# Optimization experiments

Hardware: AMD Instinct MI355X
Metric: run time of the kernel (lower is better)

The kernel has to match this reference:

```python
import jax, jax.numpy as jnp
import numpy as np
from math import sqrt

C = 64        # res_channels
LAYERS = 30
CYCLE = 10
T = 1000
B = 16
L = 32768


def setup_inputs() -> dict:
    key = jax.random.key(0)
    ks = jax.random.split(key, 12)

    def p(k, shape):
        return jax.random.normal(k, shape, dtype=jnp.float32) * 0.05

    # DiffusionEmbedding._build_embedding(T+1): table[s, 2d] = cos(s*10^(4d/63)), table[s,2d+1]=sin(...)
    steps = np.arange(T + 1, dtype=np.float64)[:, None]           # [T+1, 1]
    ang = steps * 10.0 ** (np.arange(64)[None, :] * 4.0 / 63.0)   # [T+1, 64]
    emb_table = jnp.asarray(
        np.stack([np.cos(ang), np.sin(ang)], axis=-1).reshape(T + 1, 128),
        dtype=jnp.float32,
    )

    return {
        "audio": jax.random.normal(ks[0], (B, L), dtype=jnp.float32),
        "diffusion_step": jax.random.randint(ks[1], (B,), 0, T),
        "emb_table": emb_table,                      # [T+1, 128]
        "W1": p(ks[2], (512, 128)), "b1": jnp.zeros((512,), jnp.float32),
        "W2": p(ks[3], (512, 512)), "b2": jnp.zeros((512,), jnp.float32),
        "Win": p(ks[4], (C,)),      "bin_": jnp.zeros((C,), jnp.float32),   # 1x1 conv 1->C
        "diff_W": p(ks[5], (LAYERS, C, 512)),   "diff_b": jnp.zeros((LAYERS, C), jnp.float32),
        "dconv_W": p(ks[6], (LAYERS, 2 * C, C, 3)), "dconv_b": jnp.zeros((LAYERS, 2 * C), jnp.float32),
        "out_W": p(ks[7], (LAYERS, 2 * C, C)),  "out_b": jnp.zeros((LAYERS, 2 * C), jnp.float32),
        "Wo1": p(ks[8], (C, C)),    "bo1": jnp.zeros((C,), jnp.float32),
        "Wo2": p(ks[9], (1, C)),    "bo2": jnp.zeros((1,), jnp.float32),
    }


def _dilated_conv(x, w, d):
    # x: [B, C, L], w: [2C, C, 3], 'same' padding with dilation d
    return jax.lax.conv_general_dilated(
        x, w, window_strides=(1,), padding=[(d, d)], rhs_dilation=(d,),
        dimension_numbers=("NCH", "OIH", "NCH"))


def reference(audio, diffusion_step, emb_table, W1, b1, W2, b2, Win, bin_,
              diff_W, diff_b, dconv_W, dconv_b, out_W, out_b, Wo1, bo1, Wo2, bo2):
    # input projection: Conv1d(1, C, 1) + ReLU
    x = jax.nn.relu(audio[:, None, :] * Win[None, :, None] + bin_[None, :, None])  # [B, C, L]

    t = emb_table[diffusion_step]                  # [B, 128]
    t = jax.nn.silu(t @ W1.T + b1)                 # [B, 512]
    t = jax.nn.silu(t @ W2.T + b2)                 # [B, 512]

    skip = jnp.zeros_like(x)
    for i in range(LAYERS):
        d = 2 ** (i % CYCLE)
        dp = jnp.einsum("bk,ck->bc", t, diff_W[i]) + diff_b[i]          # [B, C]
        y = _dilated_conv(x + dp[:, :, None], dconv_W[i], d)
        y = y + dconv_b[i][None, :, None]                                # [B, 2C, L]
        y = jnp.tanh(y[:, :C]) * jax.nn.sigmoid(y[:, C:])                # gated activation [B, C, L]
        z = jnp.einsum("oc,bcl->bol", out_W[i], y) + out_b[i][None, :, None]  # [B, 2C, L]
        x = (x + z[:, :C]) / sqrt(2.0)
        skip = skip + z[:, C:]

    h = skip / sqrt(float(LAYERS))
    h = jax.nn.relu(jnp.einsum("oc,bcl->bol", Wo1, h) + bo1[None, :, None])
    out = jnp.einsum("oc,bcl->bol", Wo2, h) + bo2[None, :, None]         # [B, 1, L]
    return out[:, 0, :]                                                  # [B, L]
```

## Files before the change

kernel.cpp:

```cpp
#include <hip/hip_runtime.h>
#include <hip/hip_bf16.h>
#include <math.h>
#include <stdint.h>

#define NLAYERS 30
#define BB 16
#define LL 32768

#define SS 16384.0f
#define SSI (1.0f / 16384.0f)

typedef __attribute__((ext_vector_type(8))) short bf16x8;
typedef __attribute__((ext_vector_type(8))) short s16x8;
typedef __attribute__((ext_vector_type(4))) float f32x4;

__device__ inline float bf2f(ushort u) {
    union { uint i; float f; } v; v.i = ((uint)u) << 16; return v.f;
}
__device__ inline ushort f2bf(float f) {
    uint u = __float_as_uint(f);
    return (ushort)((u + 0x7FFFu + ((u >> 16) & 1u)) >> 16);
}

__global__ void emb_kernel(const int* __restrict__ step, const float* __restrict__ emb,
                           const float* __restrict__ W1, const float* __restrict__ b1,
                           const float* __restrict__ W2, const float* __restrict__ b2,
                           float* __restrict__ t_out) {
    int b = blockIdx.x, j = threadIdx.x;
    __shared__ float e[128];
    __shared__ float t1[512];
    int s = step[b];
    if (j < 128) e[j] = emb[s * 128 + j];
    __syncthreads();
    float acc = b1[j];
    const float* w = W1 + j * 128;
    for (int k = 0; k < 128; ++k) acc += w[k] * e[k];
    t1[j] = acc / (1.f + __expf(-acc));
    __syncthreads();
    float acc2 = b2[j];
    const float* w2 = W2 + j * 512;
    for (int k = 0; k < 512; ++k) acc2 += w2[k] * t1[k];
    t_out[b * 512 + j] = acc2 / (1.f + __expf(-acc2));
}

__global__ void dp_kernel(const float* __restrict__ t, const float* __restrict__ diff_W,
                          const float* __restrict__ diff_b, float* __restrict__ dp) {
    int i = blockIdx.x, b = blockIdx.y, c = threadIdx.x;
    __shared__ float ts[512];
    for (int k = c; k < 512; k += 64) ts[k] = t[b * 512 + k];
    __syncthreads();
    const float* w = diff_W + (size_t)(i * 64 + c) * 512;
    float acc = diff_b[i * 64 + c];
    for (int k = 0; k < 512; ++k) acc += w[k] * ts[k];
    dp[(i * BB + b) * 64 + c] = acc;
}

__global__ void prep_w_kernel(const float* __restrict__ dconv_W, ushort* __restrict__ wB,
                              const float* __restrict__ out_W, ushort* __restrict__ oB,
                              const float* __restrict__ Wo1, ushort* __restrict__ Wo1B) {
    int idx = blockIdx.x * 256 + threadIdx.x;
    if (idx < 30 * 8 * 6 * 512) {
        int i = idx / 24576;
        int r = idx % 24576;
        int mt = r / 3072;
        int s = (r / 512) % 6;
        int lane = (r >> 3) & 63;
        int j = r & 7;
        int o = mt * 16 + (lane & 15);
        int tap = s >> 1;
        int c = (s & 1) * 32 + (lane >> 4) * 8 + j;
        wB[idx] = f2bf(dconv_W[((size_t)(i * 128 + o) * 64 + c) * 3 + tap]);
    }
    if (idx < 30 * 8 * 2 * 512) {
        int i = idx / 8192;
        int r = idx % 8192;
        int mt = r / 1024;
        int s = (r / 512) % 2;
        int lane = (r >> 3) & 63;
        int j = r & 7;
        int o = mt * 16 + (lane & 15);
        int c = s * 32 + (lane >> 4) * 8 + j;
        oB[idx] = f2bf(out_W[(size_t)(i * 128 + o) * 64 + c]);
    }
    if (idx < 4 * 2 * 512) {
        int mt = idx / 1024;
        int s = (idx / 512) % 2;
        int lane = (idx >> 3) & 63;
        int j = idx & 7;
        int o = mt * 16 + (lane & 15);
        int c = s * 32 + (lane >> 4) * 8 + j;
        const float hscale = SSI * 0.18257418583505537115f;
        Wo1B[idx] = f2bf(Wo1[o * 64 + c] * hscale);
    }
}

__global__ void bias3_kernel(const float* __restrict__ dp, const float* __restrict__ dconv_W,
                             const float* __restrict__ dconv_b, float* __restrict__ bias3) {
    int i = blockIdx.x, b = blockIdx.y, o = threadIdx.x;
    __shared__ float sdp[64];
    if (o < 64) sdp[o] = dp[(i * BB + b) * 64 + o];
    __syncthreads();
    const float* wrow = dconv_W + (size_t)(i * 128 + o) * 192;
    float f = 0.f, lft = 0.f, rgt = 0.f;
    for (int c = 0; c < 64; ++c) {
        float w0 = wrow[c * 3 + 0], w1 = wrow[c * 3 + 1], w2 = wrow[c * 3 + 2];
        float dv = sdp[c];
        f += dv * (w0 + w1 + w2);
        lft += dv * w0;
        rgt += dv * w2;
    }
    float* dst = bias3 + (size_t)(i * BB + b) * 384;
    dst[o] = f + dconv_b[i * 128 + o];
    dst[128 + o] = lft;
    dst[256 + o] = rgt;
}

__global__ void inproj_kernel(const float* __restrict__ audio, const float* __restrict__ Win,
                              const float* __restrict__ bin_, ushort* __restrict__ x) {
    int idx = blockIdx.x * 256 + threadIdx.x;
    int c8 = idx & 7;
    int l = (idx >> 3) & (LL - 1);
    int b = idx >> 18;
    float a = audio[(size_t)b * LL + l];
    ushort us[8];
    #pragma unroll
    for (int cc = 0; cc < 8; ++cc) {
        int c = c8 * 8 + cc;
        float v = a * Win[c] + bin_[c];
        us[cc] = f2bf(v > 0.f ? v : 0.f);
    }
    ushort4* dst = (ushort4*)(x + ((size_t)b * LL + l) * 64 + c8 * 8);
    dst[0] = make_ushort4(us[0], us[1], us[2], us[3]);
    dst[1] = make_ushort4(us[4], us[5], us[6], us[7]);
}

__global__ __launch_bounds__(256) void layer_fused(
    const ushort* __restrict__ xin, ushort* __restrict__ xout, int16_t* __restrict__ skip,
    const ushort* __restrict__ wB,
    const ushort* __restrict__ oB,
    const float* __restrict__ bias3,
    const float* __restrict__ out_b,
    int d) {
    __shared__ __align__(16) ushort su[2][16][72];

    const int b = blockIdx.y;
    const int seg = blockIdx.x;
    const int tid = threadIdx.x;
    const int lane = tid & 63;
    const int p = tid >> 6;
    const int n = lane & 15;
    const int kg = lane >> 4;
    const int rlo = p * 16 + kg * 4;

    bf16x8 A0[6], A1[6], P0[2], P1[2];
    #pragma unroll
    for (int s = 0; s < 6; ++s) {
        A0[s] = *(const bf16x8*)(wB + ((size_t)(p * 6 + s) * 64 + lane) * 8);
        A1[s] = *(const bf16x8*)(wB + ((size_t)((p + 4) * 6 + s) * 64 + lane) * 8);
    }
    #pragma unroll
    for (int s = 0; s < 2; ++s) {
        P0[s] = *(const bf16x8*)(oB + ((size_t)(p * 2 + s) * 64 + lane) * 8);
        P1[s] = *(const bf16x8*)(oB + ((size_t)((p + 4) * 2 + s) * 64 + lane) * 8);
    }
    const float* bb = bias3 + (size_t)b * 384;
    f32x4 bF_lo = *(const f32x4*)(bb + rlo);
    f32x4 bF_hi = *(const f32x4*)(bb + 64 + rlo);
    f32x4 bL_lo = *(const f32x4*)(bb + 128 + rlo);
    f32x4 bL_hi = *(const f32x4*)(bb + 192 + rlo);
    f32x4 bR_lo = *(const f32x4*)(bb + 256 + rlo);
    f32x4 bR_hi = *(const f32x4*)(bb + 320 + rlo);
    f32x4 obL = *(const f32x4*)(out_b + rlo);
    f32x4 obH = *(const f32x4*)(out_b + 64 + rlo);

    const ushort* xb = xin + (size_t)b * LL * 64;
    ushort* xo = xout + (size_t)b * LL * 64;
    int16_t* sb = skip + (size_t)b * LL * 64;
    const float inv_s2 = 0.70710678118654752440f;

    for (int t = 0; t < 32; ++t) {
        const int l0 = seg * 512 + t * 16;
        bf16x8 Bf[6];
        #pragma unroll
        for (int tap = 0; tap < 3; ++tap) {
            int lx = l0 + n + (tap - 1) * d;
            bool v = (lx >= 0) && (lx < LL);
            #pragma unroll
            for (int h = 0; h < 2; ++h) {
                bf16x8 bv = {0, 0, 0, 0, 0, 0, 0, 0};
                if (v) bv = *(const bf16x8*)(xb + (size_t)lx * 64 + h * 32 + kg * 8);
                Bf[tap * 2 + h] = bv;
            }
        }
        f32x4 accL = {0.f, 0.f, 0.f, 0.f}, accH = {0.f, 0.f, 0.f, 0.f};
        #pragma unroll
        for (int s = 0; s < 6; ++s) {
            accL = __builtin_amdgcn_mfma_f32_16x16x32_bf16(A0[s], Bf[s], accL, 0, 0, 0);
            accH = __builtin_amdgcn_mfma_f32_16x16x32_bf16(A1[s], Bf[s], accH, 0, 0, 0);
        }
        int lx0 = l0 + n;
        float selL = (lx0 < d) ? 1.f : 0.f;
        float selR = (lx0 >= LL - d) ? 1.f : 0.f;
        ushort4 uq;
        #pragma unroll
        for (int j = 0; j < 4; ++j) {
            float lo = accL[j] + bF_lo[j] - selL * bL_lo[j] - selR * bR_lo[j];
            float hi = accH[j] + bF_hi[j] - selL * bL_hi[j] - selR * bR_hi[j];
            float tv = 1.f - 2.f / (1.f + __expf(2.f * lo));
            float sv = 1.f / (1.f + __expf(-hi));
            ushort q = f2bf(tv * sv);
            if (j == 0) uq.x = q;
            if (j == 1) uq.y = q;
            if (j == 2) uq.z = q;
            if (j == 3) uq.w = q;
        }
        *(ushort4*)&su[t & 1][n][rlo] = uq;
        __syncthreads();
        bf16x8 Bp[2];
        #pragma unroll
        for (int s = 0; s < 2; ++s)
            Bp[s] = *(const bf16x8*)&su[t & 1][n][s * 32 + kg * 8];
        f32x4 zL = {0.f, 0.f, 0.f, 0.f}, zH = {0.f, 0.f, 0.f, 0.f};
        #pragma unroll
        for (int s = 0; s < 2; ++s) {
            zL = __builtin_amdgcn_mfma_f32_16x16x32_bf16(P0[s], Bp[s], zL, 0, 0, 0);
            zH = __builtin_amdgcn_mfma_f32_16x16x32_bf16(P1[s], Bp[s], zH, 0, 0, 0);
        }
        size_t off = (size_t)lx0 * 64 + rlo;
        ushort4 xv = *(const ushort4*)(xb + off);
        ushort4 xn;
        xn.x = f2bf((bf2f(xv.x) + zL[0] + obL[0]) * inv_s2);
        xn.y = f2bf((bf2f(xv.y) + zL[1] + obL[1]) * inv_s2);
        xn.z = f2bf((bf2f(xv.z) + zL[2] + obL[2]) * inv_s2);
        xn.w = f2bf((bf2f(xv.w) + zL[3] + obL[3]) * inv_s2);
        *(ushort4*)(xo + off) = xn;
        short4 so = *(const short4*)(sb + off);
        short4 sn;
        float v;
        v = fminf(fmaxf((float)so.x * SSI + zH[0] + obH[0], -1.999f), 1.999f);
        sn.x = (short)__float2int_rn(v * SS);
        v = fminf(fmaxf((float)so.y * SSI + zH[1] + obH[1], -1.999f), 1.999f);
        sn.y = (short)__float2int_rn(v * SS);
        v = fminf(fmaxf((float)so.z * SSI + zH[2] + obH[2], -1.999f), 1.999f);
        sn.z = (short)__float2int_rn(v * SS);
        v = fminf(fmaxf((float)so.w * SSI + zH[3] + obH[3], -1.999f), 1.999f);
        sn.w = (short)__float2int_rn(v * SS);
        *(short4*)(sb + off) = sn;
    }
}

__global__ __launch_bounds__(256) void head_mfma(const int16_t* __restrict__ skip,
                                                 const ushort* __restrict__ Wo1B,
                                                 const float* __restrict__ bo1,
                                                 const float* __restrict__ Wo2,
                                                 const float* __restrict__ bo2,
                                                 float* __restrict__ out) {
    const int b = blockIdx.y;
    const int seg = blockIdx.x;
    const int tid = threadIdx.x;
    const int lane = tid & 63;
    const int w = tid >> 6;
    const int n = lane & 15;
    const int kg = lane >> 4;

    bf16x8 A[4][2];
    #pragma unroll
    for (int mt = 0; mt < 4; ++mt)
        #pragma unroll
        for (int s = 0; s < 2; ++s)
            A[mt][s] = *(const bf16x8*)(Wo1B + ((size_t)(mt * 2 + s) * 64 + lane) * 8);
    f32x4 bo1v[4], wo2v[4];
    #pragma unroll
    for (int mt = 0; mt < 4; ++mt) {
        bo1v[mt] = *(const f32x4*)(bo1 + mt * 16 + kg * 4);
        wo2v[mt] = *(const f32x4*)(Wo2 + mt * 16 + kg * 4);
    }
    const float bo2v = bo2[0];
    const int16_t* sb = skip + (size_t)b * LL * 64;

    for (int t = 0; t < 16; ++t) {
        const int l0 = seg * 1024 + t * 64 + w * 16;
        bf16x8 BH[2], BL[2];
        #pragma unroll
        for (int s = 0; s < 2; ++s) {
            s16x8 v = *(const s16x8*)(sb + (size_t)(l0 + n) * 64 + s * 32 + kg * 8);
            bf16x8 bh, bl;
            #pragma unroll
            for (int e = 0; e < 8; ++e) {
                int sv = (int)v[e];
                int h8 = sv >> 8;
                int l8 = sv - (h8 << 8);
                bh[e] = (short)f2bf((float)h8);
                bl[e] = (short)f2bf((float)l8);
            }
            BH[s] = bh;
            BL[s] = bl;
        }
        f32x4 aH[4], aL[4];
        #pragma unroll
        for (int mt = 0; mt < 4; ++mt) {
            aH[mt] = (f32x4){0.f, 0.f, 0.f, 0.f};
            aL[mt] = (f32x4){0.f, 0.f, 0.f, 0.f};
            #pragma unroll
            for (int s = 0; s < 2; ++s) {
                aH[mt] = __builtin_amdgcn_mfma_f32_16x16x32_bf16(A[mt][s], BH[s], aH[mt], 0, 0, 0);
                aL[mt] = __builtin_amdgcn_mfma_f32_16x16x32_bf16(A[mt][s], BL[s], aL[mt], 0, 0, 0);
            }
        }
        float partial = 0.f;
        #pragma unroll
        for (int mt = 0; mt < 4; ++mt) {
            #pragma unroll
            for (int j = 0; j < 4; ++j) {
                float h = aH[mt][j] * 256.f + aL[mt][j] + bo1v[mt][j];
                partial += (h > 0.f ? h : 0.f) * wo2v[mt][j];
            }
        }
        partial += __shfl_xor(partial, 16, 64);
        partial += __shfl_xor(partial, 32, 64);
        if (kg == 0) out[(size_t)b * LL + l0 + n] = partial + bo2v;
    }
}

extern "C" void kernel_launch(void* const* d_in, const int* in_sizes, int n_in,
                              void* d_out, int out_size, void* d_ws, size_t ws_size,
                              hipStream_t stream) {
    const float* audio = (const float*)d_in[0];
    const int* dstep = (const int*)d_in[1];
    const float* emb = (const float*)d_in[2];
    const float* W1 = (const float*)d_in[3];
    const float* b1 = (const float*)d_in[4];
    const float* W2 = (const float*)d_in[5];
    const float* b2 = (const float*)d_in[6];
    const float* Win = (const float*)d_in[7];
    const float* bin_ = (const float*)d_in[8];
    const float* diff_W = (const float*)d_in[9];
    const float* diff_b = (const float*)d_in[10];
    const float* dconv_W = (const float*)d_in[11];
    const float* dconv_b = (const float*)d_in[12];
    const float* out_W = (const float*)d_in[13];
    const float* out_b = (const float*)d_in[14];
    const float* Wo1 = (const float*)d_in[15];
    const float* bo1 = (const float*)d_in[16];
    const float* Wo2 = (const float*)d_in[17];
    const float* bo2 = (const float*)d_in[18];

    const size_t NACT = (size_t)BB * LL * 64;

    uint8_t* p = (uint8_t*)d_ws;
    ushort* x0 = (ushort*)p;     p += NACT * 2;
    ushort* x1 = (ushort*)p;     p += NACT * 2;
    int16_t* skip = (int16_t*)p; p += NACT * 2;
    float* t = (float*)p;        p += 8192 * 4;
    float* dp = (float*)p;       p += 30720 * 4;
    float* bias3 = (float*)p;    p += 184320 * 4;
    ushort* wB = (ushort*)p;     p += 737280 * 2;
    ushort* oB = (ushort*)p;     p += 245760 * 2;
    ushort* Wo1B = (ushort*)p;   p += 4096 * 2;

    hipMemsetAsync(skip, 0, NACT * 2, stream);
    emb_kernel<<<BB, 512, 0, stream>>>(dstep, emb, W1, b1, W2, b2, t);
    dp_kernel<<<dim3(NLAYERS, BB), 64, 0, stream>>>(t, diff_W, diff_b, dp);
    prep_w_kernel<<<2880, 256, 0, stream>>>(dconv_W, wB, out_W, oB, Wo1, Wo1B);
    bias3_kernel<<<dim3(NLAYERS, BB), 128, 0, stream>>>(dp, dconv_W, dconv_b, bias3);
    inproj_kernel<<<16384, 256, 0, stream>>>(audio, Win, bin_, x0);

    dim3 lgrid(LL / 512, BB);
    ushort* xin = x0;
    ushort* xout = x1;
    for (int i = 0; i < NLAYERS; ++i) {
        int d = 1 << (i % 10);
        layer_fused<<<lgrid, 256, 0, stream>>>(
            xin, xout, skip, wB + (size_t)i * 24576, oB + (size_t)i * 8192,
            bias3 + (size_t)i * BB * 384, out_b + i * 128, d);
        ushort* tmp = xin; xin = xout; xout = tmp;
    }
    head_mfma<<<dim3(LL / 1024, BB), 256, 0, stream>>>(skip, Wo1B, bo1, Wo2, bo2,
                                                       (float*)d_out);
}
```

Baseline: 5.272 ms.

## Software-pipeline layer loads with double buffering and halve segment length

```diff
diff --git a/kernel.cpp b/kernel.cpp
--- a/kernel.cpp
+++ b/kernel.cpp
@@ -6,6 +6,8 @@
 #define NLAYERS 30
 #define BB 16
 #define LL 32768
+#define SEG 256
+#define NT (SEG / 16)
 
 #define SS 16384.0f
 #define SSI (1.0f / 16384.0f)
@@ -178,75 +180,101 @@
     int16_t* sb = skip + (size_t)b * LL * 64;
     const float inv_s2 = 0.70710678118654752440f;
 
-    for (int t = 0; t < 32; ++t) {
-        const int l0 = seg * 512 + t * 16;
-        bf16x8 Bf[6];
-        #pragma unroll
-        for (int tap = 0; tap < 3; ++tap) {
-            int lx = l0 + n + (tap - 1) * d;
-            bool v = (lx >= 0) && (lx < LL);
-            #pragma unroll
-            for (int h = 0; h < 2; ++h) {
-                bf16x8 bv = {0, 0, 0, 0, 0, 0, 0, 0};
-                if (v) bv = *(const bf16x8*)(xb + (size_t)lx * 64 + h * 32 + kg * 8);
-                Bf[tap * 2 + h] = bv;
-            }
-        }
-        f32x4 accL = {0.f, 0.f, 0.f, 0.f}, accH = {0.f, 0.f, 0.f, 0.f};
-        #pragma unroll
-        for (int s = 0; s < 6; ++s) {
-            accL = __builtin_amdgcn_mfma_f32_16x16x32_bf16(A0[s], Bf[s], accL, 0, 0, 0);
-            accH = __builtin_amdgcn_mfma_f32_16x16x32_bf16(A1[s], Bf[s], accH, 0, 0, 0);
-        }
-        int lx0 = l0 + n;
-        float selL = (lx0 < d) ? 1.f : 0.f;
-        float selR = (lx0 >= LL - d) ? 1.f : 0.f;
-        ushort4 uq;
-        #pragma unroll
-        for (int j = 0; j < 4; ++j) {
-            float lo = accL[j] + bF_lo[j] - selL * bL_lo[j] - selR * bR_lo[j];
-            float hi = accH[j] + bF_hi[j] - selL * bL_hi[j] - selR * bR_hi[j];
-            float tv = 1.f - 2.f / (1.f + __expf(2.f * lo));
-            float sv = 1.f / (1.f + __expf(-hi));
-            ushort q = f2bf(tv * sv);
-            if (j == 0) uq.x = q;
-            if (j == 1) uq.y = q;
-            if (j == 2) uq.z = q;
-            if (j == 3) uq.w = q;
-        }
-        *(ushort4*)&su[t & 1][n][rlo] = uq;
-        __syncthreads();
-        bf16x8 Bp[2];
-        #pragma unroll
-        for (int s = 0; s < 2; ++s)
-            Bp[s] = *(const bf16x8*)&su[t & 1][n][s * 32 + kg * 8];
-        f32x4 zL = {0.f, 0.f, 0.f, 0.f}, zH = {0.f, 0.f, 0.f, 0.f};
-        #pragma unroll
-        for (int s = 0; s < 2; ++s) {
-            zL = __builtin_amdgcn_mfma_f32_16x16x32_bf16(P0[s], Bp[s], zL, 0, 0, 0);
-            zH = __builtin_amdgcn_mfma_f32_16x16x32_bf16(P1[s], Bp[s], zH, 0, 0, 0);
-        }
-        size_t off = (size_t)lx0 * 64 + rlo;
-        ushort4 xv = *(const ushort4*)(xb + off);
-        ushort4 xn;
-        xn.x = f2bf((bf2f(xv.x) + zL[0] + obL[0]) * inv_s2);
-        xn.y = f2bf((bf2f(xv.y) + zL[1] + obL[1]) * inv_s2);
-        xn.z = f2bf((bf2f(xv.z) + zL[2] + obL[2]) * inv_s2);
-        xn.w = f2bf((bf2f(xv.w) + zL[3] + obL[3]) * inv_s2);
-        *(ushort4*)(xo + off) = xn;
-        short4 so = *(const short4*)(sb + off);
-        short4 sn;
-        float v;
-        v = fminf(fmaxf((float)so.x * SSI + zH[0] + obH[0], -1.999f), 1.999f);
-        sn.x = (short)__float2int_rn(v * SS);
-        v = fminf(fmaxf((float)so.y * SSI + zH[1] + obH[1], -1.999f), 1.999f);
-        sn.y = (short)__float2int_rn(v * SS);
-        v = fminf(fmaxf((float)so.z * SSI + zH[2] + obH[2], -1.999f), 1.999f);
-        sn.z = (short)__float2int_rn(v * SS);
-        v = fminf(fmaxf((float)so.w * SSI + zH[3] + obH[3], -1.999f), 1.999f);
-        sn.w = (short)__float2int_rn(v * SS);
-        *(short4*)(sb + off) = sn;
-    }
+#define LOADB(DST, TT)                                                           \
+    {                                                                            \
+        const int l0_ = seg * SEG + (TT) * 16;                                   \
+        _Pragma("unroll")                                                        \
+        for (int tap = 0; tap < 3; ++tap) {                                      \
+            int lx = l0_ + n + (tap - 1) * d;                                    \
+            bool v = (lx >= 0) && (lx < LL);                                     \
+            _Pragma("unroll")                                                    \
+            for (int h = 0; h < 2; ++h) {                                        \
+                bf16x8 bv = {0, 0, 0, 0, 0, 0, 0, 0};                            \
+                if (v) bv = *(const bf16x8*)(xb + (size_t)lx * 64 + h * 32 + kg * 8); \
+                DST[tap * 2 + h] = bv;                                           \
+            }                                                                    \
+        }                                                                        \
+    }
+
+#define LOADE(XV, SO, TT)                                                        \
+    {                                                                            \
+        size_t off_ = (size_t)(seg * SEG + (TT) * 16 + n) * 64 + rlo;            \
+        XV = *(const ushort4*)(xb + off_);                                       \
+        SO = *(const short4*)(sb + off_);                                        \
+    }
+
+#define BODY(TT, BUF, BF, XV, SO)                                                \
+    {                                                                            \
+        f32x4 accL = {0.f, 0.f, 0.f, 0.f}, accH = {0.f, 0.f, 0.f, 0.f};          \
+        _Pragma("unroll")                                                        \
+        for (int s = 0; s < 6; ++s) {                                            \
+            accL = __builtin_amdgcn_mfma_f32_16x16x32_bf16(A0[s], BF[s], accL, 0, 0, 0); \
+            accH = __builtin_amdgcn_mfma_f32_16x16x32_bf16(A1[s], BF[s], accH, 0, 0, 0); \
+        }                                                                        \
+        const int lx0 = seg * SEG + (TT) * 16 + n;                               \
+        float selL = (lx0 < d) ? 1.f : 0.f;                                      \
+        float selR = (lx0 >= LL - d) ? 1.f : 0.f;                                \
+        ushort4 uq;                                                              \
+        _Pragma("unroll")                                                        \
+        for (int j = 0; j < 4; ++j) {                                            \
+            float lo = accL[j] + bF_lo[j] - selL * bL_lo[j] - selR * bR_lo[j];   \
+            float hi = accH[j] + bF_hi[j] - selL * bL_hi[j] - selR * bR_hi[j];   \
+            float tv = 1.f - 2.f / (1.f + __expf(2.f * lo));                     \
+            float sv = 1.f / (1.f + __expf(-hi));                                \
+            ushort q = f2bf(tv * sv);                                            \
+            if (j == 0) uq.x = q;                                                \
+            if (j == 1) uq.y = q;                                                \
+            if (j == 2) uq.z = q;                                                \
+            if (j == 3) uq.w = q;                                                \
+        }                                                                        \
+        *(ushort4*)&su[BUF][n][rlo] = uq;                                        \
+        asm volatile("s_waitcnt lgkmcnt(0)" ::: "memory");                       \
+        __builtin_amdgcn_s_barrier();                                            \
+        asm volatile("" ::: "memory");                                           \
+        bf16x8 Bp0 = *(const bf16x8*)&su[BUF][n][kg * 8];                        \
+        bf16x8 Bp1 = *(const bf16x8*)&su[BUF][n][32 + kg * 8];                   \
+        f32x4 zL = {0.f, 0.f, 0.f, 0.f}, zH = {0.f, 0.f, 0.f, 0.f};              \
+        zL = __builtin_amdgcn_mfma_f32_16x16x32_bf16(P0[0], Bp0, zL, 0, 0, 0);   \
+        zH = __builtin_amdgcn_mfma_f32_16x16x32_bf16(P1[0], Bp0, zH, 0, 0, 0);   \
+        zL = __builtin_amdgcn_mfma_f32_16x16x32_bf16(P0[1], Bp1, zL, 0, 0, 0);   \
+        zH = __builtin_amdgcn_mfma_f32_16x16x32_bf16(P1[1], Bp1, zH, 0, 0, 0);   \
+        size_t off = (size_t)lx0 * 64 + rlo;                                     \
+        ushort4 xn;                                                              \
+        xn.x = f2bf((bf2f(XV.x) + zL[0] + obL[0]) * inv_s2);                     \
+        xn.y = f2bf((bf2f(XV.y) + zL[1] + obL[1]) * inv_s2);                     \
+        xn.z = f2bf((bf2f(XV.z) + zL[2] + obL[2]) * inv_s2);                     \
+        xn.w = f2bf((bf2f(XV.w) + zL[3] + obL[3]) * inv_s2);                     \
+        *(ushort4*)(xo + off) = xn;                                              \
+        short4 sn;                                                               \
+        float v;                                                                 \
+        v = fminf(fmaxf((float)SO.x * SSI + zH[0] + obH[0], -1.999f), 1.999f);   \
+        sn.x = (short)__float2int_rn(v * SS);                                    \
+        v = fminf(fmaxf((float)SO.y * SSI + zH[1] + obH[1], -1.999f), 1.999f);   \
+        sn.y = (short)__float2int_rn(v * SS);                                    \
+        v = fminf(fmaxf((float)SO.z * SSI + zH[2] + obH[2], -1.999f), 1.999f);   \
+        sn.z = (short)__float2int_rn(v * SS);                                    \
+        v = fminf(fmaxf((float)SO.w * SSI + zH[3] + obH[3], -1.999f), 1.999f);   \
+        sn.w = (short)__float2int_rn(v * SS);                                    \
+        *(short4*)(sb + off) = sn;                                               \
+    }
+
+    bf16x8 FA[6], FB[6];
+    ushort4 xvA, xvB;
+    short4 soA, soB;
+    LOADB(FA, 0)
+    LOADE(xvA, soA, 0)
+    for (int t = 0; t < NT; t += 2) {
+        LOADB(FB, t + 1)
+        LOADE(xvB, soB, t + 1)
+        BODY(t, 0, FA, xvA, soA)
+        const int tn = (t + 2 < NT) ? t + 2 : NT - 2;
+        LOADB(FA, tn)
+        LOADE(xvA, soA, tn)
+        BODY(t + 1, 1, FB, xvB, soB)
+    }
+#undef LOADB
+#undef LOADE
+#undef BODY
 }
 
 __global__ __launch_bounds__(256) void head_mfma(const int16_t* __restrict__ skip,
@@ -365,7 +393,7 @@
     bias3_kernel<<<dim3(NLAYERS, BB), 128, 0, stream>>>(dp, dconv_W, dconv_b, bias3);
     inproj_kernel<<<16384, 256, 0, stream>>>(audio, Win, bin_, x0);
 
-    dim3 lgrid(LL / 512, BB);
+    dim3 lgrid(LL / SEG, BB);
     ushort* xin = x0;
     ushort* xout = x1;
     for (int i = 0; i < NLAYERS; ++i) {
```

Measured after the change: 4.478 ms. -15.1%, faster.
